# Optimization experiments

Hardware: AMD Instinct MI355X
Metric: run time of the kernel (lower is better)

The kernel has to match this reference:

```python
import jax, jax.numpy as jnp
import numpy as np

N_LVL = [131072, 32768, 8192, 2048, 512, 256]  # active voxels per pyramid level
B = 8          # point clouds in batch
K = 27         # 3x3x3 kernel offsets
SLOPE = 0.01   # LeakyReLU default negative slope
EPS = 1e-5     # BatchNorm eps


def _bn(x, g, b):
    # MinkowskiBatchNorm, training-mode forward: stats over all points
    m = x.mean(0)
    v = x.var(0)
    return (x - m) * jax.lax.rsqrt(v + EPS) * g + b


def _lrelu(x):
    return jnp.where(x >= 0, x, SLOPE * x)


def _lin_block(x, w, g, b):
    # MinkowskiLinear(bias=False) + BN + LeakyReLU (also models 1x1 conv)
    return _lrelu(_bn(x @ w, g, b))


def _conv_block(x, nbr, w, g, b):
    # sparse conv as gather-GEMM: [N,K,Cin] x [K,Cin,Cout] -> [N,Cout]
    y = jnp.einsum('nkc,kco->no', x[nbr], w)
    return _lrelu(_bn(y, g, b))


def _maxpool(x, pmap):
    # stride-2 kernel-3 sparse max pool via precomputed pooling map
    return x[pmap].max(axis=1)


def setup_inputs() -> dict:
    key = jax.random.key(0)
    ks = iter(jax.random.split(key, 80))

    def nrm(shape, scale):
        return jax.random.normal(next(ks), shape, dtype=jnp.float32) * jnp.float32(scale)

    inp = {}
    inp['x'] = nrm((N_LVL[0], 3), 1.0)
    inp['w_mlp1'] = nrm((3, 16), 1.0 / np.sqrt(3.0))
    inp['g_mlp1'] = jnp.ones(16, jnp.float32)
    inp['b_mlp1'] = jnp.zeros(16, jnp.float32)
    conv_dims = [(16, 32), (32, 48), (48, 96), (96, 128), (128, 256), (256, 512)]
    down_dims = [(48, 32), (80, 48), (144, 96), (224, 128), (384, 256)]
    for i, (ci, co) in enumerate(conv_dims):
        inp[f'w_c{i+1}'] = nrm((K, ci, co), np.sqrt(2.0 / (K * co)))  # kaiming fan_out
        inp[f'g_c{i+1}'] = jnp.ones(co, jnp.float32)
        inp[f'b_c{i+1}'] = jnp.zeros(co, jnp.float32)
    for i, (ci, co) in enumerate(down_dims):
        inp[f'w_d{i+1}'] = nrm((ci, co), np.sqrt(2.0 / co))
        inp[f'g_d{i+1}'] = jnp.ones(co, jnp.float32)
        inp[f'b_d{i+1}'] = jnp.zeros(co, jnp.float32)
    inp['w_f1'] = nrm((1024, 512), 1.0 / 32.0)
    inp['g_f1'] = jnp.ones(512, jnp.float32)
    inp['b_f1'] = jnp.zeros(512, jnp.float32)
    inp['w_f2'] = nrm((512, 256), 1.0 / np.sqrt(512.0))
    inp['g_f2'] = jnp.ones(256, jnp.float32)
    inp['b_f2'] = jnp.zeros(256, jnp.float32)
    inp['w_f3'] = nrm((256, 20), 1.0 / 16.0)
    inp['bias_f3'] = jnp.zeros(20, jnp.float32)
    for i in range(6):
        inp[f'nbr{i}'] = jax.random.randint(next(ks), (N_LVL[i], K), 0, N_LVL[i], dtype=jnp.int32)
    for i in range(1, 6):
        inp[f'pool{i}'] = jax.random.randint(next(ks), (N_LVL[i], K), 0, N_LVL[i - 1], dtype=jnp.int32)
    inp['batch5'] = jnp.repeat(jnp.arange(B, dtype=jnp.int32), N_LVL[5] // B)
    return inp


def reference(x, w_mlp1, g_mlp1, b_mlp1,
              w_c1, g_c1, b_c1, w_c2, g_c2, b_c2, w_c3, g_c3, b_c3,
              w_c4, g_c4, b_c4, w_c5, g_c5, b_c5, w_c6, g_c6, b_c6,
              w_d1, g_d1, b_d1, w_d2, g_d2, b_d2, w_d3, g_d3, b_d3,
              w_d4, g_d4, b_d4, w_d5, g_d5, b_d5,
              w_f1, g_f1, b_f1, w_f2, g_f2, b_f2, w_f3, bias_f3,
              nbr0, nbr1, nbr2, nbr3, nbr4, nbr5,
              pool1, pool2, pool3, pool4, pool5, batch5):
    convs = [(w_c1, g_c1, b_c1), (w_c2, g_c2, b_c2), (w_c3, g_c3, b_c3),
             (w_c4, g_c4, b_c4), (w_c5, g_c5, b_c5)]
    downs = [(w_d1, g_d1, b_d1), (w_d2, g_d2, b_d2), (w_d3, g_d3, b_d3),
             (w_d4, g_d4, b_d4), (w_d5, g_d5, b_d5)]
    nbrs = [nbr0, nbr1, nbr2, nbr3, nbr4]
    pools = [pool1, pool2, pool3, pool4, pool5]

    y = _lin_block(x, w_mlp1, g_mlp1, b_mlp1)  # mlp1, level 0
    for i in range(5):  # fixed 5 conv/cat/down/pool stages (structural loop)
        out = _conv_block(y, nbrs[i], *convs[i])
        y = _lin_block(jnp.concatenate([y, out], axis=1), *downs[i])  # cat + down (1x1)
        y = _maxpool(y, pools[i])
    y = _conv_block(y, nbr5, w_c6, g_c6, b_c6)  # conv6 at level 5: [N5, 512]

    xmax = jax.ops.segment_max(y, batch5, num_segments=B)
    cnt = jax.ops.segment_sum(jnp.ones((y.shape[0], 1), y.dtype), batch5, num_segments=B)
    xavg = jax.ops.segment_sum(y, batch5, num_segments=B) / cnt
    z = jnp.concatenate([xmax, xavg], axis=1)  # [B, 1024]

    z = _lin_block(z, w_f1, g_f1, b_f1)  # dropout = identity (eval)
    z = _lin_block(z, w_f2, g_f2, b_f2)
    return z @ w_f3 + bias_f3  # [B, 20] logits
```

## Files before the change

kernel.cpp:

```cpp
#include <hip/hip_runtime.h>
#include <math.h>

#define BN_EPS 1e-5f


__device__ __forceinline__ void fma4(float s, const float4& w, float4& a) {
    a.x = fmaf(s, w.x, a.x);
    a.y = fmaf(s, w.y, a.y);
    a.z = fmaf(s, w.z, a.z);
    a.w = fmaf(s, w.w, a.w);
}

__device__ __forceinline__ float nlr(float x, float sc, float sh) {
    float t = fmaf(x, sc, sh);
    return fmaxf(t, 0.01f * t);
}

__device__ __forceinline__ void bn_coef(const float* __restrict__ sums,
                                        const float* __restrict__ g,
                                        const float* __restrict__ b,
                                        int C, int c, float inv_n,
                                        float& sc, float& sh) {
    float mean = sums[c] * inv_n;
    float var = fmaxf(fmaf(-mean, mean, sums[C + c] * inv_n), 0.f);
    sc = g[c] * rsqrtf(var + BN_EPS);
    sh = fmaf(-mean, sc, b[c]);
}

__global__ void zero_kernel(float* __restrict__ p, int n) {
    int i = blockIdx.x * blockDim.x + threadIdx.x;
    if (i < n) p[i] = 0.f;
}

__global__ void mlp1_kernel(const float* __restrict__ x, const float* __restrict__ w,
                            float* __restrict__ out, int N) {
    int n = blockIdx.x * blockDim.x + threadIdx.x;
    if (n >= N) return;
    float x0 = x[n * 3], x1 = x[n * 3 + 1], x2 = x[n * 3 + 2];
    #pragma unroll
    for (int c4 = 0; c4 < 4; c4++) {
        float4 w0 = *reinterpret_cast<const float4*>(w + 0 + c4 * 4);
        float4 w1 = *reinterpret_cast<const float4*>(w + 16 + c4 * 4);
        float4 w2 = *reinterpret_cast<const float4*>(w + 32 + c4 * 4);
        float4 o;
        o.x = fmaf(x0, w0.x, fmaf(x1, w1.x, x2 * w2.x));
        o.y = fmaf(x0, w0.y, fmaf(x1, w1.y, x2 * w2.y));
        o.z = fmaf(x0, w0.z, fmaf(x1, w1.z, x2 * w2.z));
        o.w = fmaf(x0, w0.w, fmaf(x1, w1.w, x2 * w2.w));
        *reinterpret_cast<float4*>(out + n * 16 + c4 * 4) = o;
    }
}

__global__ void stats4_kernel(const float4* __restrict__ x, int total4, int C, int C4,
                              float* __restrict__ sums) {
    __shared__ float ls[1024];
    int tid = threadIdx.x;
    for (int j = tid; j < 2 * C; j += blockDim.x) ls[j] = 0.f;
    __syncthreads();
    int stride = gridDim.x * blockDim.x;
    int i = blockIdx.x * blockDim.x + tid;
    int c4 = i % C4;
    float4 s = make_float4(0.f, 0.f, 0.f, 0.f);
    float4 q = make_float4(0.f, 0.f, 0.f, 0.f);
    for (; i < total4; i += stride) {
        float4 v = x[i];
        s.x += v.x; s.y += v.y; s.z += v.z; s.w += v.w;
        q.x = fmaf(v.x, v.x, q.x); q.y = fmaf(v.y, v.y, q.y);
        q.z = fmaf(v.z, v.z, q.z); q.w = fmaf(v.w, v.w, q.w);
    }
    int cb = c4 * 4;
    atomicAdd(&ls[cb + 0], s.x); atomicAdd(&ls[cb + 1], s.y);
    atomicAdd(&ls[cb + 2], s.z); atomicAdd(&ls[cb + 3], s.w);
    atomicAdd(&ls[C + cb + 0], q.x); atomicAdd(&ls[C + cb + 1], q.y);
    atomicAdd(&ls[C + cb + 2], q.z); atomicAdd(&ls[C + cb + 3], q.w);
    __syncthreads();
    for (int j = tid; j < 2 * C; j += blockDim.x) atomicAdd(&sums[j], ls[j]);
}

template <int C, int KS>
__global__ __launch_bounds__(256) void reducek_kernel(
    const float4* __restrict__ in, float4* __restrict__ out, int total4,
    float* __restrict__ sums) {
    __shared__ float ls[1024];
    constexpr int C4 = C / 4;
    int tid = threadIdx.x;
    for (int j = tid; j < 2 * C; j += blockDim.x) ls[j] = 0.f;
    __syncthreads();
    int stride = gridDim.x * blockDim.x;
    int i = blockIdx.x * blockDim.x + tid;
    int c4 = i % C4;
    float4 s = make_float4(0.f, 0.f, 0.f, 0.f);
    float4 q = make_float4(0.f, 0.f, 0.f, 0.f);
    for (; i < total4; i += stride) {
        float4 v = make_float4(0.f, 0.f, 0.f, 0.f);
        #pragma unroll
        for (int p = 0; p < KS; p++) {
            float4 t = in[(size_t)p * total4 + i];
            v.x += t.x; v.y += t.y; v.z += t.z; v.w += t.w;
        }
        out[i] = v;
        s.x += v.x; s.y += v.y; s.z += v.z; s.w += v.w;
        q.x = fmaf(v.x, v.x, q.x); q.y = fmaf(v.y, v.y, q.y);
        q.z = fmaf(v.z, v.z, q.z); q.w = fmaf(v.w, v.w, q.w);
    }
    int cb = c4 * 4;
    atomicAdd(&ls[cb + 0], s.x); atomicAdd(&ls[cb + 1], s.y);
    atomicAdd(&ls[cb + 2], s.z); atomicAdd(&ls[cb + 3], s.w);
    atomicAdd(&ls[C + cb + 0], q.x); atomicAdd(&ls[C + cb + 1], q.y);
    atomicAdd(&ls[C + cb + 2], q.z); atomicAdd(&ls[C + cb + 3], q.w);
    __syncthreads();
    for (int j = tid; j < 2 * C; j += blockDim.x) atomicAdd(&sums[j], ls[j]);
}

template <int CIN, int COUT, int CO_TILE, int NCOT, int MT, int TM, int NTHR,
          int NQ, int KT, bool NORM_IN, bool STATS>
__global__ __launch_bounds__(NTHR) void convd_kernel(
    const float* __restrict__ y, const int* __restrict__ nbr,
    const float* __restrict__ w, float* __restrict__ out,
    const float* __restrict__ s_in, const float* __restrict__ g_in,
    const float* __restrict__ b_in, float inv_n,
    float* __restrict__ s_out) {
    constexpr int CQT = CO_TILE / (4 * NQ);
    constexpr int MGRP = NTHR / CQT;
    constexpr int RT = TM / MGRP;
    static_assert(MGRP * RT == TM, "tile mismatch");

    __shared__ float nsc[NORM_IN ? CIN : 1];
    __shared__ float nsh[NORM_IN ? CIN : 1];
    __shared__ float sred[STATS ? 2 * CO_TILE : 1];

    const int tid = threadIdx.x;
    const int bid = blockIdx.x;
    const int cot = bid % NCOT;
    const int rest = bid / NCOT;
    const int mt = rest % MT;
    const int ks = rest / MT;
    const int m0 = mt * TM;
    const int cobase = cot * CO_TILE;
    const int k0 = ks * KT;
    const int cq = tid % CQT;
    const int mg = tid / CQT;

    if constexpr (NORM_IN) {
        for (int c = tid; c < CIN; c += NTHR) {
            float sc, sh;
            bn_coef(s_in, g_in, b_in, CIN, c, inv_n, sc, sh);
            nsc[c] = sc;
            nsh[c] = sh;
        }
        __syncthreads();
    }

    int mrow[RT];
    #pragma unroll
    for (int r = 0; r < RT; r++) mrow[r] = m0 + mg + r * MGRP;

    float4 acc[RT][NQ];
    #pragma unroll
    for (int r = 0; r < RT; r++)
        #pragma unroll
        for (int q = 0; q < NQ; q++) acc[r][q] = make_float4(0.f, 0.f, 0.f, 0.f);

    for (int kk = k0; kk < k0 + KT; kk++) {
        int rows[RT];
        #pragma unroll
        for (int r = 0; r < RT; r++) rows[r] = nbr[(size_t)mrow[r] * 27 + kk];
        const float* wk = w + (size_t)kk * CIN * COUT + cobase + cq * (4 * NQ);
        #pragma unroll 4
        for (int ci4 = 0; ci4 < CIN / 4; ci4++) {
            float4 yv[RT];
            #pragma unroll
            for (int r = 0; r < RT; r++)
                yv[r] = *reinterpret_cast<const float4*>(
                    y + (size_t)rows[r] * CIN + ci4 * 4);
            if constexpr (NORM_IN) {
                float4 sc = *reinterpret_cast<const float4*>(&nsc[ci4 * 4]);
                float4 sh = *reinterpret_cast<const float4*>(&nsh[ci4 * 4]);
                #pragma unroll
                for (int r = 0; r < RT; r++) {
                    yv[r].x = nlr(yv[r].x, sc.x, sh.x);
                    yv[r].y = nlr(yv[r].y, sc.y, sh.y);
                    yv[r].z = nlr(yv[r].z, sc.z, sh.z);
                    yv[r].w = nlr(yv[r].w, sc.w, sh.w);
                }
            }
            #pragma unroll
            for (int jj = 0; jj < 4; jj++) {
                #pragma unroll
                for (int q = 0; q < NQ; q++) {
                    float4 wv = *reinterpret_cast<const float4*>(
                        wk + (size_t)(ci4 * 4 + jj) * COUT + q * 4);
                    #pragma unroll
                    for (int r = 0; r < RT; r++) {
                        float e = jj == 0 ? yv[r].x : jj == 1 ? yv[r].y
                                 : jj == 2 ? yv[r].z : yv[r].w;
                        fma4(e, wv, acc[r][q]);
                    }
                }
            }
        }
    }

    float* outp = out + (size_t)ks * MT * TM * COUT;
    #pragma unroll
    for (int r = 0; r < RT; r++)
        #pragma unroll
        for (int q = 0; q < NQ; q++)
            *reinterpret_cast<float4*>(
                outp + (size_t)mrow[r] * COUT + cobase + cq * (4 * NQ) + q * 4) =
                acc[r][q];

    if constexpr (STATS) {
        for (int j = tid; j < 2 * CO_TILE; j += NTHR) sred[j] = 0.f;
        __syncthreads();
        #pragma unroll
        for (int q = 0; q < NQ; q++) {
            float4 s = make_float4(0.f, 0.f, 0.f, 0.f);
            float4 qq = make_float4(0.f, 0.f, 0.f, 0.f);
            #pragma unroll
            for (int r = 0; r < RT; r++) {
                float4 v = acc[r][q];
                s.x += v.x; s.y += v.y; s.z += v.z; s.w += v.w;
                qq.x = fmaf(v.x, v.x, qq.x); qq.y = fmaf(v.y, v.y, qq.y);
                qq.z = fmaf(v.z, v.z, qq.z); qq.w = fmaf(v.w, v.w, qq.w);
            }
            int cb = cq * (4 * NQ) + q * 4;
            atomicAdd(&sred[cb + 0], s.x); atomicAdd(&sred[cb + 1], s.y);
            atomicAdd(&sred[cb + 2], s.z); atomicAdd(&sred[cb + 3], s.w);
            atomicAdd(&sred[CO_TILE + cb + 0], qq.x);
            atomicAdd(&sred[CO_TILE + cb + 1], qq.y);
            atomicAdd(&sred[CO_TILE + cb + 2], qq.z);
            atomicAdd(&sred[CO_TILE + cb + 3], qq.w);
        }
        __syncthreads();
        for (int j = tid; j < CO_TILE; j += NTHR) {
            atomicAdd(&s_out[cobase + j], sred[j]);
            atomicAdd(&s_out[COUT + cobase + j], sred[CO_TILE + j]);
        }
    }
}

template <int C1, int C2, int COUT, int NQ, int NTHR, bool NORM1>
__global__ __launch_bounds__(NTHR) void down3_kernel(
    const float* __restrict__ in1, const float* __restrict__ in2,
    const float* __restrict__ w, float* __restrict__ out,
    const float* __restrict__ s1, const float* __restrict__ g1,
    const float* __restrict__ b1, float inv1,
    const float* __restrict__ s2, const float* __restrict__ g2,
    const float* __restrict__ b2, float inv2,
    float* __restrict__ s_out) {
    constexpr int CQT = COUT / (4 * NQ);
    constexpr int PAIRS = NTHR / CQT;
    __shared__ __align__(16) float n1c[C1], n1h[C1], n2c[C2], n2h[C2];
    __shared__ float sred[2 * COUT];

    const int tid = threadIdx.x;
    if constexpr (NORM1) {
        for (int c = tid; c < C1; c += NTHR) {
            float sc, sh;
            bn_coef(s1, g1, b1, C1, c, inv1, sc, sh);
            n1c[c] = sc; n1h[c] = sh;
        }
    }
    for (int c = tid; c < C2; c += NTHR) {
        float sc, sh;
        bn_coef(s2, g2, b2, C2, c, inv2, sc, sh);
        n2c[c] = sc; n2h[c] = sh;
    }
    for (int j = tid; j < 2 * COUT; j += NTHR) sred[j] = 0.f;
    __syncthreads();

    const int cq = tid % CQT;
    const int pr = tid / CQT;
    const int n0 = (blockIdx.x * PAIRS + pr) * 2;

    float4 acc[2][NQ];
    #pragma unroll
    for (int r = 0; r < 2; r++)
        #pragma unroll
        for (int q = 0; q < NQ; q++) acc[r][q] = make_float4(0.f, 0.f, 0.f, 0.f);

    const float* w1 = w + cq * (4 * NQ);
    #pragma unroll 8
    for (int ci4 = 0; ci4 < C1 / 4; ci4++) {
        float4 a0 = *reinterpret_cast<const float4*>(in1 + (size_t)n0 * C1 + ci4 * 4);
        float4 a1 = *reinterpret_cast<const float4*>(in1 + (size_t)(n0 + 1) * C1 + ci4 * 4);
        if constexpr (NORM1) {
            float4 sc = *reinterpret_cast<const float4*>(&n1c[ci4 * 4]);
            float4 sh = *reinterpret_cast<const float4*>(&n1h[ci4 * 4]);
            a0.x = nlr(a0.x, sc.x, sh.x); a0.y = nlr(a0.y, sc.y, sh.y);
            a0.z = nlr(a0.z, sc.z, sh.z); a0.w = nlr(a0.w, sc.w, sh.w);
            a1.x = nlr(a1.x, sc.x, sh.x); a1.y = nlr(a1.y, sc.y, sh.y);
            a1.z = nlr(a1.z, sc.z, sh.z); a1.w = nlr(a1.w, sc.w, sh.w);
        }
        #pragma unroll
        for (int jj = 0; jj < 4; jj++) {
            const float* wp = w1 + (size_t)(ci4 * 4 + jj) * COUT;
            float e0 = jj == 0 ? a0.x : jj == 1 ? a0.y : jj == 2 ? a0.z : a0.w;
            float e1 = jj == 0 ? a1.x : jj == 1 ? a1.y : jj == 2 ? a1.z : a1.w;
            #pragma unroll
            for (int q = 0; q < NQ; q++) {
                float4 wv = *reinterpret_cast<const float4*>(wp + q * 4);
                fma4(e0, wv, acc[0][q]);
                fma4(e1, wv, acc[1][q]);
            }
        }
    }
    const float* w2 = w + (size_t)C1 * COUT + cq * (4 * NQ);
    #pragma unroll 8
    for (int ci4 = 0; ci4 < C2 / 4; ci4++) {
        float4 a0 = *reinterpret_cast<const float4*>(in2 + (size_t)n0 * C2 + ci4 * 4);
        float4 a1 = *reinterpret_cast<const float4*>(in2 + (size_t)(n0 + 1) * C2 + ci4 * 4);
        float4 sc = *reinterpret_cast<const float4*>(&n2c[ci4 * 4]);
        float4 sh = *reinterpret_cast<const float4*>(&n2h[ci4 * 4]);
        a0.x = nlr(a0.x, sc.x, sh.x); a0.y = nlr(a0.y, sc.y, sh.y);
        a0.z = nlr(a0.z, sc.z, sh.z); a0.w = nlr(a0.w, sc.w, sh.w);
        a1.x = nlr(a1.x, sc.x, sh.x); a1.y = nlr(a1.y, sc.y, sh.y);
        a1.z = nlr(a1.z, sc.z, sh.z); a1.w = nlr(a1.w, sc.w, sh.w);
        #pragma unroll
        for (int jj = 0; jj < 4; jj++) {
            const float* wp = w2 + (size_t)(ci4 * 4 + jj) * COUT;
            float e0 = jj == 0 ? a0.x : jj == 1 ? a0.y : jj == 2 ? a0.z : a0.w;
            float e1 = jj == 0 ? a1.x : jj == 1 ? a1.y : jj == 2 ? a1.z : a1.w;
            #pragma unroll
            for (int q = 0; q < NQ; q++) {
                float4 wv = *reinterpret_cast<const float4*>(wp + q * 4);
                fma4(e0, wv, acc[0][q]);
                fma4(e1, wv, acc[1][q]);
            }
        }
    }
    #pragma unroll
    for (int r = 0; r < 2; r++)
        #pragma unroll
        for (int q = 0; q < NQ; q++)
            *reinterpret_cast<float4*>(out + (size_t)(n0 + r) * COUT + cq * (4 * NQ) + q * 4) =
                acc[r][q];

    #pragma unroll
    for (int q = 0; q < NQ; q++) {
        float4 s = make_float4(0.f, 0.f, 0.f, 0.f);
        float4 qq = make_float4(0.f, 0.f, 0.f, 0.f);
        #pragma unroll
        for (int r = 0; r < 2; r++) {
            float4 v = acc[r][q];
            s.x += v.x; s.y += v.y; s.z += v.z; s.w += v.w;
            qq.x = fmaf(v.x, v.x, qq.x); qq.y = fmaf(v.y, v.y, qq.y);
            qq.z = fmaf(v.z, v.z, qq.z); qq.w = fmaf(v.w, v.w, qq.w);
        }
        int cb = cq * (4 * NQ) + q * 4;
        atomicAdd(&sred[cb + 0], s.x); atomicAdd(&sred[cb + 1], s.y);
        atomicAdd(&sred[cb + 2], s.z); atomicAdd(&sred[cb + 3], s.w);
        atomicAdd(&sred[COUT + cb + 0], qq.x);
        atomicAdd(&sred[COUT + cb + 1], qq.y);
        atomicAdd(&sred[COUT + cb + 2], qq.z);
        atomicAdd(&sred[COUT + cb + 3], qq.w);
    }
    __syncthreads();
    for (int j = tid; j < COUT; j += NTHR) {
        atomicAdd(&s_out[j], sred[j]);
        atomicAdd(&s_out[COUT + j], sred[COUT + j]);
    }
}

template <int C, int NTHR>
__global__ __launch_bounds__(NTHR) void pool2_kernel(
    const float* __restrict__ draw, const int* __restrict__ pmap,
    const float* __restrict__ sums, const float* __restrict__ g,
    const float* __restrict__ b, float inv_n,
    float* __restrict__ yout, int Nout) {
    constexpr int C4 = C / 4;
    int i = blockIdx.x * NTHR + threadIdx.x;
    if (i >= Nout * C4) return;
    int n = i / C4, c4 = i % C4;
    float sc[4], sh[4];
    #pragma unroll
    for (int j = 0; j < 4; j++) bn_coef(sums, g, b, C, c4 * 4 + j, inv_n, sc[j], sh[j]);
// ... 94 lines not shown
        red[kg * 520 + (coq * 4 + 2) * 8 + n] = acc[n].z;
        red[kg * 520 + (coq * 4 + 3) * 8 + n] = acc[n].w;
    }
    __syncthreads();
    for (int oi = tid; oi < 512; oi += 256) {
        int c = oi >> 3;
        int n = oi & 7;
        float s = 0.f;
        #pragma unroll
        for (int gg = 0; gg < 16; gg++) s += red[gg * 520 + c * 8 + n];
        float* op = out + (size_t)n * COUT + cobase + c;
        if (KSPLIT > 1) atomicAdd(op, s);
        else *op = s;
    }
}

__global__ void f3n_kernel(const float* __restrict__ in, const float* __restrict__ w,
                           const float* __restrict__ bias,
                           const float* __restrict__ sums, const float* __restrict__ g,
                           const float* __restrict__ b, float inv_n,
                           float* __restrict__ out) {
    __shared__ float zin[8 * 256];
    int tid = threadIdx.x;
    for (int idx = tid; idx < 2048; idx += 256) {
        int c = idx & 255;
        float sc, sh;
        bn_coef(sums, g, b, 256, c, inv_n, sc, sh);
        zin[idx] = nlr(in[idx], sc, sh);
    }
    __syncthreads();
    if (tid >= 160) return;
    int n = tid / 20, co = tid % 20;
    float acc = bias[co];
    for (int ci = 0; ci < 256; ci++)
        acc = fmaf(zin[n * 256 + ci], w[ci * 20 + co], acc);
    out[tid] = acc;
}


extern "C" void kernel_launch(void* const* d_in, const int* in_sizes, int n_in,
                              void* d_out, int out_size, void* d_ws, size_t ws_size,
                              hipStream_t stream) {
    (void)in_sizes; (void)n_in; (void)out_size; (void)ws_size;

    const int N0 = 131072, N1 = 32768, N2 = 8192, N3 = 2048, N4 = 512, N5 = 256;

    const float* x      = (const float*)d_in[0];
    const float* w_mlp1 = (const float*)d_in[1];
    const float* g_mlp1 = (const float*)d_in[2];
    const float* b_mlp1 = (const float*)d_in[3];
    const float* w_c[6]; const float* g_c[6]; const float* b_c[6];
    for (int i = 0; i < 6; i++) {
        w_c[i] = (const float*)d_in[4 + 3 * i];
        g_c[i] = (const float*)d_in[5 + 3 * i];
        b_c[i] = (const float*)d_in[6 + 3 * i];
    }
    const float* w_d[5]; const float* g_d[5]; const float* b_d[5];
    for (int i = 0; i < 5; i++) {
        w_d[i] = (const float*)d_in[22 + 3 * i];
        g_d[i] = (const float*)d_in[23 + 3 * i];
        b_d[i] = (const float*)d_in[24 + 3 * i];
    }
    const float* w_f1 = (const float*)d_in[37];
    const float* g_f1 = (const float*)d_in[38];
    const float* b_f1 = (const float*)d_in[39];
    const float* w_f2 = (const float*)d_in[40];
    const float* g_f2 = (const float*)d_in[41];
    const float* b_f2 = (const float*)d_in[42];
    const float* w_f3 = (const float*)d_in[43];
    const float* bias_f3 = (const float*)d_in[44];
    const int* nbr[6];
    for (int i = 0; i < 6; i++) nbr[i] = (const int*)d_in[45 + i];
    const int* pool[5];
    for (int i = 0; i < 5; i++) pool[i] = (const int*)d_in[51 + i];

    float* ws    = (float*)d_ws;
    float* bufA  = ws;
    float* bufB  = bufA + 2097152;
    float* bufC  = bufB + 4194304;
    float* stats = bufC + 4194304;
    float* out = (float*)d_out;

    auto st = [&](int slot) { return stats + slot * 1024; };
    auto run_stats = [&](const float* buf, int total, int C, int bs, int slot) {
        int total4 = total / 4, C4 = C / 4;
        int gr = (total4 + bs - 1) / bs;
        if (gr > 768) gr = 768;
        stats4_kernel<<<gr, bs, 0, stream>>>((const float4*)buf, total4, C, C4, st(slot));
    };

    const float iN0 = 1.f / N0, iN1 = 1.f / N1, iN2 = 1.f / N2, iN3 = 1.f / N3,
                iN4 = 1.f / N4, iN5 = 1.f / N5, i8 = 1.f / 8.f;

    zero_kernel<<<56, 256, 0, stream>>>(stats, 14 * 1024);

    mlp1_kernel<<<N0 / 256, 256, 0, stream>>>(x, w_mlp1, bufA, N0);
    run_stats(bufA, N0 * 16, 16, 256, 0);

    convd_kernel<16, 32, 32, 1, 1024, 128, 256, 2, 27, true, true>
        <<<1024, 256, 0, stream>>>(bufA, nbr[0], w_c[0], bufB,
                                   st(0), g_mlp1, b_mlp1, iN0, st(1));
    down3_kernel<16, 32, 32, 2, 256, true>
        <<<1024, 256, 0, stream>>>(bufA, bufB, w_d[0], bufC,
                                   st(0), g_mlp1, b_mlp1, iN0,
                                   st(1), g_c[0], b_c[0], iN0, st(2));
    pool2_kernel<32, 256><<<N1 * 8 / 256, 256, 0, stream>>>(
        bufC, pool[0], st(2), g_d[0], b_d[0], iN0, bufA, N1);

    convd_kernel<32, 48, 48, 1, 512, 64, 192, 2, 27, false, true>
        <<<512, 192, 0, stream>>>(bufA, nbr[1], w_c[1], bufB,
                                  nullptr, nullptr, nullptr, 0.f, st(3));
    down3_kernel<32, 48, 48, 2, 192, false>
        <<<512, 192, 0, stream>>>(bufA, bufB, w_d[1], bufC,
                                  nullptr, nullptr, nullptr, 0.f,
                                  st(3), g_c[1], b_c[1], iN1, st(4));
    pool2_kernel<48, 192><<<N2 * 12 / 192, 192, 0, stream>>>(
        bufC, pool[1], st(4), g_d[1], b_d[1], iN1, bufA, N2);

    convd_kernel<48, 96, 48, 2, 128, 64, 192, 2, 27, false, true>
        <<<256, 192, 0, stream>>>(bufA, nbr[2], w_c[2], bufB,
                                  nullptr, nullptr, nullptr, 0.f, st(5));
    down3_kernel<48, 96, 96, 2, 192, false>
        <<<256, 192, 0, stream>>>(bufA, bufB, w_d[2], bufC,
                                  nullptr, nullptr, nullptr, 0.f,
                                  st(5), g_c[2], b_c[2], iN2, st(6));
    pool2_kernel<96, 192><<<N3 * 24 / 192, 192, 0, stream>>>(
        bufC, pool[2], st(6), g_d[2], b_d[2], iN2, bufA, N3);

    convd_kernel<96, 128, 64, 2, 32, 64, 256, 2, 3, false, false>
        <<<576, 256, 0, stream>>>(bufA, nbr[3], w_c[3], bufC,
                                  nullptr, nullptr, nullptr, 0.f, nullptr);
    reducek_kernel<128, 9><<<256, 256, 0, stream>>>(
        (const float4*)bufC, (float4*)bufB, N3 * 32, st(7));
    down3_kernel<96, 128, 128, 2, 256, false>
        <<<64, 256, 0, stream>>>(bufA, bufB, w_d[3], bufC,
                                 nullptr, nullptr, nullptr, 0.f,
                                 st(7), g_c[3], b_c[3], iN3, st(8));
    pool2_kernel<128, 256><<<N4 * 32 / 256, 256, 0, stream>>>(
        bufC, pool[3], st(8), g_d[3], b_d[3], iN3, bufA, N4);

    convd_kernel<128, 256, 64, 4, 8, 64, 256, 2, 3, false, false>
        <<<288, 256, 0, stream>>>(bufA, nbr[4], w_c[4], bufC,
                                  nullptr, nullptr, nullptr, 0.f, nullptr);
    reducek_kernel<256, 9><<<128, 256, 0, stream>>>(
        (const float4*)bufC, (float4*)bufB, N4 * 64, st(9));
    down3_kernel<128, 256, 256, 2, 256, false>
        <<<32, 256, 0, stream>>>(bufA, bufB, w_d[4], bufC,
                                 nullptr, nullptr, nullptr, 0.f,
                                 st(9), g_c[4], b_c[4], iN4, st(10));
    pool2_kernel<256, 256><<<N5 * 64 / 256, 256, 0, stream>>>(
        bufC, pool[4], st(10), g_d[4], b_d[4], iN4, bufA, N5);

    convd_kernel<256, 512, 64, 8, 4, 64, 256, 2, 1, false, false>
        <<<864, 256, 0, stream>>>(bufA, nbr[5], w_c[5], bufC,
                                  nullptr, nullptr, nullptr, 0.f, nullptr);
    reducek_kernel<512, 27><<<128, 256, 0, stream>>>(
        (const float4*)bufC, (float4*)bufB, N5 * 128, st(11));

    segpool2_kernel<<<8, 512, 0, stream>>>(bufB, st(11), g_c[5], b_c[5], iN5, bufC);

    zero_kernel<<<16, 256, 0, stream>>>(bufA, 4096);
    fc_kernel<1024, 512, 4, false><<<dim3(8, 4), 256, 0, stream>>>(
        bufC, w_f1, nullptr, nullptr, nullptr, 0.f, bufA);
    run_stats(bufA, 8 * 512, 512, 256, 12);

    zero_kernel<<<8, 256, 0, stream>>>(bufB, 2048);
    fc_kernel<512, 256, 4, true><<<dim3(4, 4), 256, 0, stream>>>(
        bufA, w_f2, st(12), g_f1, b_f1, i8, bufB);
    run_stats(bufB, 8 * 256, 256, 256, 13);

    f3n_kernel<<<1, 256, 0, stream>>>(bufB, w_f3, bias_f3, st(13), g_f2, b_f2, i8, out);
}
```

Before: 1.148 ms.

## Split-K sparse convs more widely and double-buffer gathers in first conv

The level-1 and level-2 convolutions now split the 27 kernel offsets across more blocks, writing per-split partial outputs that a reducek kernel sums while also computing BN statistics. The deeper convolutions move to one offset per block with a 27-way reduction, done in place in bufB. The first convolution gains a prefetch path that loads the next offset's gathered rows while FMAs run on the current ones. Neighbour indices are also loaded one offset ahead. The aim is more parallelism on under-occupied layers and hidden gather latency, at the cost of extra partial-sum memory traffic and larger intermediate buffers.

After: 1.055 ms. -8.2%, faster.

```diff
diff --git a/kernel.cpp b/kernel.cpp
--- a/kernel.cpp
+++ b/kernel.cpp
@@ -78,9 +78,8 @@
 }
 
 template <int C, int KS>
-__global__ __launch_bounds__(256) void reducek_kernel(
-    const float4* __restrict__ in, float4* __restrict__ out, int total4,
-    float* __restrict__ sums) {
+__global__ void reducek_kernel(const float4* __restrict__ in, float4* __restrict__ out,
+                               int total4, float* __restrict__ sums) {
     __shared__ float ls[1024];
     constexpr int C4 = C / 4;
     int tid = threadIdx.x;
@@ -113,7 +112,7 @@
 }
 
 template <int CIN, int COUT, int CO_TILE, int NCOT, int MT, int TM, int NTHR,
-          int NQ, int KT, bool NORM_IN, bool STATS>
+          int NQ, int KT, bool NORM_IN, bool STATS, bool PREF>
 __global__ __launch_bounds__(NTHR) void convd_kernel(
     const float* __restrict__ y, const int* __restrict__ nbr,
     const float* __restrict__ w, float* __restrict__ out,
@@ -123,7 +122,9 @@
     constexpr int CQT = CO_TILE / (4 * NQ);
     constexpr int MGRP = NTHR / CQT;
     constexpr int RT = TM / MGRP;
+    constexpr int C4N = CIN / 4;
     static_assert(MGRP * RT == TM, "tile mismatch");
+    static_assert(MGRP * CQT == NTHR, "thread mismatch");
 
     __shared__ float nsc[NORM_IN ? CIN : 1];
     __shared__ float nsh[NORM_IN ? CIN : 1];
@@ -148,7 +149,6 @@
             nsc[c] = sc;
             nsh[c] = sh;
         }
-        __syncthreads();
     }
 
     int mrow[RT];
@@ -161,43 +161,93 @@
         #pragma unroll
         for (int q = 0; q < NQ; q++) acc[r][q] = make_float4(0.f, 0.f, 0.f, 0.f);
 
-    for (int kk = k0; kk < k0 + KT; kk++) {
-        int rows[RT];
-        #pragma unroll
-        for (int r = 0; r < RT; r++) rows[r] = nbr[(size_t)mrow[r] * 27 + kk];
-        const float* wk = w + (size_t)kk * CIN * COUT + cobase + cq * (4 * NQ);
-        #pragma unroll 4
-        for (int ci4 = 0; ci4 < CIN / 4; ci4++) {
-            float4 yv[RT];
-            #pragma unroll
-            for (int r = 0; r < RT; r++)
-                yv[r] = *reinterpret_cast<const float4*>(
-                    y + (size_t)rows[r] * CIN + ci4 * 4);
-            if constexpr (NORM_IN) {
-                float4 sc = *reinterpret_cast<const float4*>(&nsc[ci4 * 4]);
-                float4 sh = *reinterpret_cast<const float4*>(&nsh[ci4 * 4]);
+    auto ldidx = [&](int k, int (&rr)[RT]) {
+        #pragma unroll
+        for (int r = 0; r < RT; r++) rr[r] = nbr[(size_t)mrow[r] * 27 + k];
+    };
+    auto fma_ci4 = [&](const float* wk, int ci4, float4 (&yv)[RT]) {
+        if constexpr (NORM_IN) {
+            float4 sc = *reinterpret_cast<const float4*>(&nsc[ci4 * 4]);
+            float4 sh = *reinterpret_cast<const float4*>(&nsh[ci4 * 4]);
+            #pragma unroll
+            for (int r = 0; r < RT; r++) {
+                yv[r].x = nlr(yv[r].x, sc.x, sh.x);
+                yv[r].y = nlr(yv[r].y, sc.y, sh.y);
+                yv[r].z = nlr(yv[r].z, sc.z, sh.z);
+                yv[r].w = nlr(yv[r].w, sc.w, sh.w);
+            }
+        }
+        #pragma unroll
+        for (int jj = 0; jj < 4; jj++) {
+            #pragma unroll
+            for (int q = 0; q < NQ; q++) {
+                float4 wv = *reinterpret_cast<const float4*>(
+                    wk + (size_t)(ci4 * 4 + jj) * COUT + q * 4);
                 #pragma unroll
                 for (int r = 0; r < RT; r++) {
-                    yv[r].x = nlr(yv[r].x, sc.x, sh.x);
-                    yv[r].y = nlr(yv[r].y, sc.y, sh.y);
-                    yv[r].z = nlr(yv[r].z, sc.z, sh.z);
-                    yv[r].w = nlr(yv[r].w, sc.w, sh.w);
+                    float e = jj == 0 ? yv[r].x : jj == 1 ? yv[r].y
+                             : jj == 2 ? yv[r].z : yv[r].w;
+                    fma4(e, wv, acc[r][q]);
                 }
             }
-            #pragma unroll
-            for (int jj = 0; jj < 4; jj++) {
+        }
+    };
+
+    if constexpr (PREF) {
+        auto ldy = [&](const int (&rr)[RT], float4 (&yv)[RT][C4N]) {
+            #pragma unroll
+            for (int r = 0; r < RT; r++)
                 #pragma unroll
-                for (int q = 0; q < NQ; q++) {
-                    float4 wv = *reinterpret_cast<const float4*>(
-                        wk + (size_t)(ci4 * 4 + jj) * COUT + q * 4);
-                    #pragma unroll
-                    for (int r = 0; r < RT; r++) {
-                        float e = jj == 0 ? yv[r].x : jj == 1 ? yv[r].y
-                                 : jj == 2 ? yv[r].z : yv[r].w;
-                        fma4(e, wv, acc[r][q]);
-                    }
-                }
-            }
+                for (int c4 = 0; c4 < C4N; c4++)
+                    yv[r][c4] = *reinterpret_cast<const float4*>(
+                        y + (size_t)rr[r] * CIN + c4 * 4);
+        };
+        auto fmak = [&](int k, float4 (&yv)[RT][C4N]) {
+            const float* wk = w + (size_t)k * CIN * COUT + cobase + cq * (4 * NQ);
+            #pragma unroll
+            for (int ci4 = 0; ci4 < C4N; ci4++) {
+                float4 col[RT];
+                #pragma unroll
+                for (int r = 0; r < RT; r++) col[r] = yv[r][ci4];
+                fma_ci4(wk, ci4, col);
+            }
+        };
+        int ra[RT], rb[RT];
+        float4 ya[RT][C4N], yb[RT][C4N];
+        ldidx(k0, ra);
+        ldy(ra, ya);
+        if constexpr (NORM_IN) __syncthreads();
+        int kk = 0;
+        for (; kk + 2 <= KT; kk += 2) {
+            ldidx(k0 + kk + 1, rb);
+            ldy(rb, yb);
+            fmak(k0 + kk, ya);
+            if (kk + 2 < KT) {
+                ldidx(k0 + kk + 2, ra);
+                ldy(ra, ya);
+            }
+            fmak(k0 + kk + 1, yb);
+        }
+        if (KT & 1) fmak(k0 + KT - 1, ya);
+    } else {
+        if constexpr (NORM_IN) __syncthreads();
+        int rows[RT];
+        ldidx(k0, rows);
+        for (int kk = k0; kk < k0 + KT; kk++) {
+            int rnext[RT];
+            if (kk + 1 < k0 + KT) ldidx(kk + 1, rnext);
+            const float* wk = w + (size_t)kk * CIN * COUT + cobase + cq * (4 * NQ);
+            #pragma unroll 4
+            for (int ci4 = 0; ci4 < C4N; ci4++) {
+                float4 yv[RT];
+                #pragma unroll
+                for (int r = 0; r < RT; r++)
+                    yv[r] = *reinterpret_cast<const float4*>(
+                        y + (size_t)rows[r] * CIN + ci4 * 4);
+                fma_ci4(wk, ci4, yv);
+            }
+            #pragma unroll
+            for (int r = 0; r < RT; r++) rows[r] = rnext[r];
         }
     }
 
@@ -568,7 +618,7 @@
     mlp1_kernel<<<N0 / 256, 256, 0, stream>>>(x, w_mlp1, bufA, N0);
     run_stats(bufA, N0 * 16, 16, 256, 0);
 
-    convd_kernel<16, 32, 32, 1, 1024, 128, 256, 2, 27, true, true>
+    convd_kernel<16, 32, 32, 1, 1024, 128, 256, 2, 27, true, true, true>
         <<<1024, 256, 0, stream>>>(bufA, nbr[0], w_c[0], bufB,
                                    st(0), g_mlp1, b_mlp1, iN0, st(1));
     down3_kernel<16, 32, 32, 2, 256, true>
@@ -578,9 +628,11 @@
     pool2_kernel<32, 256><<<N1 * 8 / 256, 256, 0, stream>>>(
         bufC, pool[0], st(2), g_d[0], b_d[0], iN0, bufA, N1);
 
-    convd_kernel<32, 48, 48, 1, 512, 64, 192, 2, 27, false, true>
-        <<<512, 192, 0, stream>>>(bufA, nbr[1], w_c[1], bufB,
-                                  nullptr, nullptr, nullptr, 0.f, st(3));
+    convd_kernel<32, 48, 48, 1, 512, 64, 192, 2, 9, false, false, false>
+        <<<1536, 192, 0, stream>>>(bufA, nbr[1], w_c[1], bufB,
+                                   nullptr, nullptr, nullptr, 0.f, nullptr);
+    reducek_kernel<48, 3><<<1024, 192, 0, stream>>>(
+        (const float4*)bufB, (float4*)bufB, N1 * 12, st(3));
     down3_kernel<32, 48, 48, 2, 192, false>
         <<<512, 192, 0, stream>>>(bufA, bufB, w_d[1], bufC,
                                   nullptr, nullptr, nullptr, 0.f,
@@ -588,9 +640,11 @@
     pool2_kernel<48, 192><<<N2 * 12 / 192, 192, 0, stream>>>(
         bufC, pool[1], st(4), g_d[1], b_d[1], iN1, bufA, N2);
 
-    convd_kernel<48, 96, 48, 2, 128, 64, 192, 2, 27, false, true>
-        <<<256, 192, 0, stream>>>(bufA, nbr[2], w_c[2], bufB,
-                                  nullptr, nullptr, nullptr, 0.f, st(5));
+    convd_kernel<48, 96, 48, 2, 128, 64, 192, 2, 3, false, false, false>
+        <<<2304, 192, 0, stream>>>(bufA, nbr[2], w_c[2], bufB,
+                                   nullptr, nullptr, nullptr, 0.f, nullptr);
+    reducek_kernel<96, 9><<<1024, 192, 0, stream>>>(
+        (const float4*)bufB, (float4*)bufB, N2 * 24, st(5));
     down3_kernel<48, 96, 96, 2, 192, false>
         <<<256, 192, 0, stream>>>(bufA, bufB, w_d[2], bufC,
                                   nullptr, nullptr, nullptr, 0.f,
@@ -598,11 +652,11 @@
     pool2_kernel<96, 192><<<N3 * 24 / 192, 192, 0, stream>>>(
         bufC, pool[2], st(6), g_d[2], b_d[2], iN2, bufA, N3);
 
-    convd_kernel<96, 128, 64, 2, 32, 64, 256, 2, 3, false, false>
-        <<<576, 256, 0, stream>>>(bufA, nbr[3], w_c[3], bufC,
-                                  nullptr, nullptr, nullptr, 0.f, nullptr);
-    reducek_kernel<128, 9><<<256, 256, 0, stream>>>(
-        (const float4*)bufC, (float4*)bufB, N3 * 32, st(7));
+    convd_kernel<96, 128, 64, 2, 32, 64, 256, 2, 1, false, false, false>
+        <<<1728, 256, 0, stream>>>(bufA, nbr[3], w_c[3], bufB,
+                                   nullptr, nullptr, nullptr, 0.f, nullptr);
+    reducek_kernel<128, 27><<<256, 256, 0, stream>>>(
+        (const float4*)bufB, (float4*)bufB, N3 * 32, st(7));
     down3_kernel<96, 128, 128, 2, 256, false>
         <<<64, 256, 0, stream>>>(bufA, bufB, w_d[3], bufC,
                                  nullptr, nullptr, nullptr, 0.f,
@@ -610,11 +664,11 @@
     pool2_kernel<128, 256><<<N4 * 32 / 256, 256, 0, stream>>>(
         bufC, pool[3], st(8), g_d[3], b_d[3], iN3, bufA, N4);
 
-    convd_kernel<128, 256, 64, 4, 8, 64, 256, 2, 3, false, false>
-        <<<288, 256, 0, stream>>>(bufA, nbr[4], w_c[4], bufC,
+    convd_kernel<128, 256, 64, 4, 8, 64, 256, 2, 1, false, false, false>
+        <<<864, 256, 0, stream>>>(bufA, nbr[4], w_c[4], bufB,
                                   nullptr, nullptr, nullptr, 0.f, nullptr);
-    reducek_kernel<256, 9><<<128, 256, 0, stream>>>(
-        (const float4*)bufC, (float4*)bufB, N4 * 64, st(9));
+    reducek_kernel<256, 27><<<128, 256, 0, stream>>>(
+        (const float4*)bufB, (float4*)bufB, N4 * 64, st(9));
     down3_kernel<128, 256, 256, 2, 256, false>
         <<<32, 256, 0, stream>>>(bufA, bufB, w_d[4], bufC,
                                  nullptr, nullptr, nullptr, 0.f,
@@ -622,11 +676,11 @@
     pool2_kernel<256, 256><<<N5 * 64 / 256, 256, 0, stream>>>(
         bufC, pool[4], st(10), g_d[4], b_d[4], iN4, bufA, N5);
 
-    convd_kernel<256, 512, 64, 8, 4, 64, 256, 2, 1, false, false>
-        <<<864, 256, 0, stream>>>(bufA, nbr[5], w_c[5], bufC,
+    convd_kernel<256, 512, 64, 8, 4, 64, 256, 2, 1, false, false, false>
+        <<<864, 256, 0, stream>>>(bufA, nbr[5], w_c[5], bufB,
                                   nullptr, nullptr, nullptr, 0.f, nullptr);
     reducek_kernel<512, 27><<<128, 256, 0, stream>>>(
-        (const float4*)bufC, (float4*)bufB, N5 * 128, st(11));
+        (const float4*)bufB, (float4*)bufB, N5 * 128, st(11));
 
     segpool2_kernel<<<8, 512, 0, stream>>>(bufB, st(11), g_c[5], b_c[5], iN5, bufC);
 
```

## Split-K and retile sparse convs, add prefetched gather path, pre-normalize level-0 features

Applied to the files above, without the earlier changes.

Level-0 features are now normalized in place by a new norm0 kernel, so the conv and down kernels no longer apply BN and LeakyReLU on the fly. A PREF path in the conv kernel preloads the neighbour indices and double-buffers whole input rows in registers across kernel offsets. All conv launches are retiled to smaller row tiles with more blocks. Conv2 and conv3 become split-K launches followed by an in-place reducek reduction, which also computes the BN statistics. The aim is more parallelism and better latency hiding on the gather-GEMMs, at the cost of extra partial-sum traffic, extra launches and higher register pressure from the row buffers.

Result: slower. 1.495 ms (+30.2%).

```diff
diff --git a/kernel.cpp b/kernel.cpp
--- a/kernel.cpp
+++ b/kernel.cpp
@@ -77,10 +77,32 @@
     for (int j = tid; j < 2 * C; j += blockDim.x) atomicAdd(&sums[j], ls[j]);
 }
 
+__global__ void norm0_kernel(float4* __restrict__ y, int total4,
+                             const float* __restrict__ sums, const float* __restrict__ g,
+                             const float* __restrict__ b, float inv_n) {
+    __shared__ float lsc[16], lsh[16];
+    int tid = threadIdx.x;
+    if (tid < 16) {
+        float sc, sh;
+        bn_coef(sums, g, b, 16, tid, inv_n, sc, sh);
+        lsc[tid] = sc;
+        lsh[tid] = sh;
+    }
+    __syncthreads();
+    int i = blockIdx.x * blockDim.x + tid;
+    if (i >= total4) return;
+    int cb = (i & 3) * 4;
+    float4 v = y[i];
+    v.x = nlr(v.x, lsc[cb + 0], lsh[cb + 0]);
+    v.y = nlr(v.y, lsc[cb + 1], lsh[cb + 1]);
+    v.z = nlr(v.z, lsc[cb + 2], lsh[cb + 2]);
+    v.w = nlr(v.w, lsc[cb + 3], lsh[cb + 3]);
+    y[i] = v;
+}
+
 template <int C, int KS>
-__global__ __launch_bounds__(256) void reducek_kernel(
-    const float4* __restrict__ in, float4* __restrict__ out, int total4,
-    float* __restrict__ sums) {
+__global__ void reducek_kernel(const float4* __restrict__ in, float4* __restrict__ out,
+                               int total4, float* __restrict__ sums) {
     __shared__ float ls[1024];
     constexpr int C4 = C / 4;
     int tid = threadIdx.x;
@@ -113,20 +135,19 @@
 }
 
 template <int CIN, int COUT, int CO_TILE, int NCOT, int MT, int TM, int NTHR,
-          int NQ, int KT, bool NORM_IN, bool STATS>
+          int NQ, int KT, bool STATS, bool PREF>
 __global__ __launch_bounds__(NTHR) void convd_kernel(
     const float* __restrict__ y, const int* __restrict__ nbr,
     const float* __restrict__ w, float* __restrict__ out,
-    const float* __restrict__ s_in, const float* __restrict__ g_in,
-    const float* __restrict__ b_in, float inv_n,
     float* __restrict__ s_out) {
     constexpr int CQT = CO_TILE / (4 * NQ);
     constexpr int MGRP = NTHR / CQT;
     constexpr int RT = TM / MGRP;
+    constexpr int C4N = CIN / 4;
     static_assert(MGRP * RT == TM, "tile mismatch");
-
-    __shared__ float nsc[NORM_IN ? CIN : 1];
-    __shared__ float nsh[NORM_IN ? CIN : 1];
+    static_assert(MGRP * CQT == NTHR, "thread mismatch");
+    static_assert(!PREF || RT == 1, "PREF requires RT==1");
+
     __shared__ float sred[STATS ? 2 * CO_TILE : 1];
 
     const int tid = threadIdx.x;
@@ -141,63 +162,91 @@
     const int cq = tid % CQT;
     const int mg = tid / CQT;
 
-    if constexpr (NORM_IN) {
-        for (int c = tid; c < CIN; c += NTHR) {
-            float sc, sh;
-            bn_coef(s_in, g_in, b_in, CIN, c, inv_n, sc, sh);
-            nsc[c] = sc;
-            nsh[c] = sh;
-        }
-        __syncthreads();
-    }
-
-    int mrow[RT];
-    #pragma unroll
-    for (int r = 0; r < RT; r++) mrow[r] = m0 + mg + r * MGRP;
-
     float4 acc[RT][NQ];
     #pragma unroll
     for (int r = 0; r < RT; r++)
         #pragma unroll
         for (int q = 0; q < NQ; q++) acc[r][q] = make_float4(0.f, 0.f, 0.f, 0.f);
 
-    for (int kk = k0; kk < k0 + KT; kk++) {
+    if constexpr (PREF) {
+        const int mrow = m0 + mg;
+        int idxs[KT];
+        #pragma unroll
+        for (int kk = 0; kk < KT; kk++)
+            idxs[kk] = nbr[(size_t)mrow * 27 + k0 + kk];
+
+        auto ldy = [&](int row, float4 (&yv)[C4N]) {
+            #pragma unroll
+            for (int c4 = 0; c4 < C4N; c4++)
+                yv[c4] = *reinterpret_cast<const float4*>(
+                    y + (size_t)row * CIN + c4 * 4);
+        };
+        auto fmak = [&](int k, const float4 (&yv)[C4N]) {
+            const float* wk = w + (size_t)k * CIN * COUT + cobase + cq * (4 * NQ);
+            #pragma unroll
+            for (int c4 = 0; c4 < C4N; c4++) {
+                #pragma unroll
+                for (int jj = 0; jj < 4; jj++) {
+                    float e = jj == 0 ? yv[c4].x : jj == 1 ? yv[c4].y
+                             : jj == 2 ? yv[c4].z : yv[c4].w;
+                    #pragma unroll
+                    for (int q = 0; q < NQ; q++) {
+                        float4 wv = *reinterpret_cast<const float4*>(
+                            wk + (size_t)(c4 * 4 + jj) * COUT + q * 4);
+                        fma4(e, wv, acc[0][q]);
+                    }
+                }
+            }
+        };
+        float4 ya[C4N], yb[C4N];
+        ldy(idxs[0], ya);
+        int kk = 0;
+        for (; kk + 2 <= KT; kk += 2) {
+            ldy(idxs[kk + 1], yb);
+            fmak(k0 + kk, ya);
+            if (kk + 2 < KT) ldy(idxs[kk + 2], ya);
+            fmak(k0 + kk + 1, yb);
+        }
+        if (KT & 1) fmak(k0 + KT - 1, ya);
+    } else {
+        int mrow[RT];
+        #pragma unroll
+        for (int r = 0; r < RT; r++) mrow[r] = m0 + mg + r * MGRP;
         int rows[RT];
         #pragma unroll
-        for (int r = 0; r < RT; r++) rows[r] = nbr[(size_t)mrow[r] * 27 + kk];
-        const float* wk = w + (size_t)kk * CIN * COUT + cobase + cq * (4 * NQ);
-        #pragma unroll 4
-        for (int ci4 = 0; ci4 < CIN / 4; ci4++) {
-            float4 yv[RT];
-            #pragma unroll
-            for (int r = 0; r < RT; r++)
-                yv[r] = *reinterpret_cast<const float4*>(
-                    y + (size_t)rows[r] * CIN + ci4 * 4);
-            if constexpr (NORM_IN) {
-                float4 sc = *reinterpret_cast<const float4*>(&nsc[ci4 * 4]);
-                float4 sh = *reinterpret_cast<const float4*>(&nsh[ci4 * 4]);
+        for (int r = 0; r < RT; r++) rows[r] = nbr[(size_t)mrow[r] * 27 + k0];
+        for (int kk = k0; kk < k0 + KT; kk++) {
+            int rnext[RT];
+            if (kk + 1 < k0 + KT) {
                 #pragma unroll
-                for (int r = 0; r < RT; r++) {
-                    yv[r].x = nlr(yv[r].x, sc.x, sh.x);
-                    yv[r].y = nlr(yv[r].y, sc.y, sh.y);
-                    yv[r].z = nlr(yv[r].z, sc.z, sh.z);
-                    yv[r].w = nlr(yv[r].w, sc.w, sh.w);
+                for (int r = 0; r < RT; r++)
+                    rnext[r] = nbr[(size_t)mrow[r] * 27 + kk + 1];
+            }
+            const float* wk = w + (size_t)kk * CIN * COUT + cobase + cq * (4 * NQ);
+            #pragma unroll 4
+            for (int c4 = 0; c4 < C4N; c4++) {
+                float4 yv[RT];
+                #pragma unroll
+                for (int r = 0; r < RT; r++)
+                    yv[r] = *reinterpret_cast<const float4*>(
+                        y + (size_t)rows[r] * CIN + c4 * 4);
+                #pragma unroll
+                for (int jj = 0; jj < 4; jj++) {
+                    #pragma unroll
+                    for (int q = 0; q < NQ; q++) {
+                        float4 wv = *reinterpret_cast<const float4*>(
+                            wk + (size_t)(c4 * 4 + jj) * COUT + q * 4);
+                        #pragma unroll
+                        for (int r = 0; r < RT; r++) {
+                            float e = jj == 0 ? yv[r].x : jj == 1 ? yv[r].y
+                                     : jj == 2 ? yv[r].z : yv[r].w;
+                            fma4(e, wv, acc[r][q]);
+                        }
+                    }
                 }
             }
             #pragma unroll
-            for (int jj = 0; jj < 4; jj++) {
-                #pragma unroll
-                for (int q = 0; q < NQ; q++) {
-                    float4 wv = *reinterpret_cast<const float4*>(
-                        wk + (size_t)(ci4 * 4 + jj) * COUT + q * 4);
-                    #pragma unroll
-                    for (int r = 0; r < RT; r++) {
-                        float e = jj == 0 ? yv[r].x : jj == 1 ? yv[r].y
-                                 : jj == 2 ? yv[r].z : yv[r].w;
-                        fma4(e, wv, acc[r][q]);
-                    }
-                }
-            }
+            for (int r = 0; r < RT; r++) rows[r] = rnext[r];
         }
     }
 
@@ -207,7 +256,7 @@
         #pragma unroll
         for (int q = 0; q < NQ; q++)
             *reinterpret_cast<float4*>(
-                outp + (size_t)mrow[r] * COUT + cobase + cq * (4 * NQ) + q * 4) =
+                outp + (size_t)(m0 + mg + r * MGRP) * COUT + cobase + cq * (4 * NQ) + q * 4) =
                 acc[r][q];
 
     if constexpr (STATS) {
@@ -240,28 +289,19 @@
     }
 }
 
-template <int C1, int C2, int COUT, int NQ, int NTHR, bool NORM1>
+template <int C1, int C2, int COUT, int NQ, int NTHR>
 __global__ __launch_bounds__(NTHR) void down3_kernel(
     const float* __restrict__ in1, const float* __restrict__ in2,
     const float* __restrict__ w, float* __restrict__ out,
-    const float* __restrict__ s1, const float* __restrict__ g1,
-    const float* __restrict__ b1, float inv1,
     const float* __restrict__ s2, const float* __restrict__ g2,
     const float* __restrict__ b2, float inv2,
     float* __restrict__ s_out) {
     constexpr int CQT = COUT / (4 * NQ);
     constexpr int PAIRS = NTHR / CQT;
-    __shared__ __align__(16) float n1c[C1], n1h[C1], n2c[C2], n2h[C2];
+    __shared__ __align__(16) float n2c[C2], n2h[C2];
     __shared__ float sred[2 * COUT];
 
     const int tid = threadIdx.x;
-    if constexpr (NORM1) {
-        for (int c = tid; c < C1; c += NTHR) {
-            float sc, sh;
-            bn_coef(s1, g1, b1, C1, c, inv1, sc, sh);
-            n1c[c] = sc; n1h[c] = sh;
-        }
-    }
     for (int c = tid; c < C2; c += NTHR) {
         float sc, sh;
         bn_coef(s2, g2, b2, C2, c, inv2, sc, sh);
@@ -285,14 +325,6 @@
     for (int ci4 = 0; ci4 < C1 / 4; ci4++) {
         float4 a0 = *reinterpret_cast<const float4*>(in1 + (size_t)n0 * C1 + ci4 * 4);
         float4 a1 = *reinterpret_cast<const float4*>(in1 + (size_t)(n0 + 1) * C1 + ci4 * 4);
-        if constexpr (NORM1) {
-            float4 sc = *reinterpret_cast<const float4*>(&n1c[ci4 * 4]);
-            float4 sh = *reinterpret_cast<const float4*>(&n1h[ci4 * 4]);
-            a0.x = nlr(a0.x, sc.x, sh.x); a0.y = nlr(a0.y, sc.y, sh.y);
-            a0.z = nlr(a0.z, sc.z, sh.z); a0.w = nlr(a0.w, sc.w, sh.w);
-            a1.x = nlr(a1.x, sc.x, sh.x); a1.y = nlr(a1.y, sc.y, sh.y);
-            a1.z = nlr(a1.z, sc.z, sh.z); a1.w = nlr(a1.w, sc.w, sh.w);
-        }
         #pragma unroll
         for (int jj = 0; jj < 4; jj++) {
             const float* wp = w1 + (size_t)(ci4 * 4 + jj) * COUT;
@@ -553,12 +585,6 @@
     float* out = (float*)d_out;
 
     auto st = [&](int slot) { return stats + slot * 1024; };
-    auto run_stats = [&](const float* buf, int total, int C, int bs, int slot) {
-        int total4 = total / 4, C4 = C / 4;
-        int gr = (total4 + bs - 1) / bs;
-        if (gr > 768) gr = 768;
-        stats4_kernel<<<gr, bs, 0, stream>>>((const float4*)buf, total4, C, C4, st(slot));
-    };
 
     const float iN0 = 1.f / N0, iN1 = 1.f / N1, iN2 = 1.f / N2, iN3 = 1.f / N3,
                 iN4 = 1.f / N4, iN5 = 1.f / N5, i8 = 1.f / 8.f;
@@ -566,79 +592,76 @@
     zero_kernel<<<56, 256, 0, stream>>>(stats, 14 * 1024);
 
     mlp1_kernel<<<N0 / 256, 256, 0, stream>>>(x, w_mlp1, bufA, N0);
-    run_stats(bufA, N0 * 16, 16, 256, 0);
-
-    convd_kernel<16, 32, 32, 1, 1024, 128, 256, 2, 27, true, true>
-        <<<1024, 256, 0, stream>>>(bufA, nbr[0], w_c[0], bufB,
-                                   st(0), g_mlp1, b_mlp1, iN0, st(1));
-    down3_kernel<16, 32, 32, 2, 256, true>
+    stats4_kernel<<<768, 256, 0, stream>>>((const float4*)bufA, N0 * 4, 16, 4, st(0));
+    norm0_kernel<<<N0 * 4 / 256, 256, 0, stream>>>(
+        (float4*)bufA, N0 * 4, st(0), g_mlp1, b_mlp1, iN0);
+
+    convd_kernel<16, 32, 32, 1, 2048, 64, 256, 2, 27, true, true>
+        <<<2048, 256, 0, stream>>>(bufA, nbr[0], w_c[0], bufB, st(1));
+    down3_kernel<16, 32, 32, 2, 256>
         <<<1024, 256, 0, stream>>>(bufA, bufB, w_d[0], bufC,
-                                   st(0), g_mlp1, b_mlp1, iN0,
                                    st(1), g_c[0], b_c[0], iN0, st(2));
     pool2_kernel<32, 256><<<N1 * 8 / 256, 256, 0, stream>>>(
         bufC, pool[0], st(2), g_d[0], b_d[0], iN0, bufA, N1);
 
-    convd_kernel<32, 48, 48, 1, 512, 64, 192, 2, 27, false, true>
-        <<<512, 192, 0, stream>>>(bufA, nbr[1], w_c[1], bufB,
-                                  nullptr, nullptr, nullptr, 0.f, st(3));
-    down3_kernel<32, 48, 48, 2, 192, false>
+    convd_kernel<32, 48, 48, 1, 1024, 32, 192, 2, 9, false, true>
+        <<<3072, 192, 0, stream>>>(bufA, nbr[1], w_c[1], bufB, nullptr);
+    reducek_kernel<48, 3><<<1024, 192, 0, stream>>>(
+        (const float4*)bufB, (float4*)bufB, N1 * 12, st(3));
+    down3_kernel<32, 48, 48, 2, 192>
         <<<512, 192, 0, stream>>>(bufA, bufB, w_d[1], bufC,
-                                  nullptr, nullptr, nullptr, 0.f,
                                   st(3), g_c[1], b_c[1], iN1, st(4));
     pool2_kernel<48, 192><<<N2 * 12 / 192, 192, 0, stream>>>(
         bufC, pool[1], st(4), g_d[1], b_d[1], iN1, bufA, N2);
 
-    convd_kernel<48, 96, 48, 2, 128, 64, 192, 2, 27, false, true>
-        <<<256, 192, 0, stream>>>(bufA, nbr[2], w_c[2], bufB,
-                                  nullptr, nullptr, nullptr, 0.f, st(5));
-    down3_kernel<48, 96, 96, 2, 192, false>
+    convd_kernel<48, 96, 48, 2, 256, 32, 192, 2, 9, false, false>
+        <<<1536, 192, 0, stream>>>(bufA, nbr[2], w_c[2], bufB, nullptr);
+    reducek_kernel<96, 3><<<1024, 192, 0, stream>>>(
+        (const float4*)bufB, (float4*)bufB, N2 * 24, st(5));
+    down3_kernel<48, 96, 96, 2, 192>
         <<<256, 192, 0, stream>>>(bufA, bufB, w_d[2], bufC,
-                                  nullptr, nullptr, nullptr, 0.f,
                                   st(5), g_c[2], b_c[2], iN2, st(6));
     pool2_kernel<96, 192><<<N3 * 24 / 192, 192, 0, stream>>>(
         bufC, pool[2], st(6), g_d[2], b_d[2], iN2, bufA, N3);
 
-    convd_kernel<96, 128, 64, 2, 32, 64, 256, 2, 3, false, false>
-        <<<576, 256, 0, stream>>>(bufA, nbr[3], w_c[3], bufC,
-                                  nullptr, nullptr, nullptr, 0.f, nullptr);
+    convd_kernel<96, 128, 64, 2, 64, 32, 256, 2, 3, false, false>
+        <<<1152, 256, 0, stream>>>(bufA, nbr[3], w_c[3], bufB, nullptr);
     reducek_kernel<128, 9><<<256, 256, 0, stream>>>(
-        (const float4*)bufC, (float4*)bufB, N3 * 32, st(7));
-    down3_kernel<96, 128, 128, 2, 256, false>
+        (const float4*)bufB, (float4*)bufB, N3 * 32, st(7));
+    down3_kernel<96, 128, 128, 2, 256>
         <<<64, 256, 0, stream>>>(bufA, bufB, w_d[3], bufC,
-                                 nullptr, nullptr, nullptr, 0.f,
                                  st(7), g_c[3], b_c[3], iN3, st(8));
     pool2_kernel<128, 256><<<N4 * 32 / 256, 256, 0, stream>>>(
         bufC, pool[3], st(8), g_d[3], b_d[3], iN3, bufA, N4);
 
-    convd_kernel<128, 256, 64, 4, 8, 64, 256, 2, 3, false, false>
-        <<<288, 256, 0, stream>>>(bufA, nbr[4], w_c[4], bufC,
-                                  nullptr, nullptr, nullptr, 0.f, nullptr);
+    convd_kernel<128, 256, 64, 4, 16, 32, 256, 2, 3, false, false>
+        <<<576, 256, 0, stream>>>(bufA, nbr[4], w_c[4], bufB, nullptr);
     reducek_kernel<256, 9><<<128, 256, 0, stream>>>(
-        (const float4*)bufC, (float4*)bufB, N4 * 64, st(9));
-    down3_kernel<128, 256, 256, 2, 256, false>
+        (const float4*)bufB, (float4*)bufB, N4 * 64, st(9));
+    down3_kernel<128, 256, 256, 2, 256>
         <<<32, 256, 0, stream>>>(bufA, bufB, w_d[4], bufC,
-                                 nullptr, nullptr, nullptr, 0.f,
                                  st(9), g_c[4], b_c[4], iN4, st(10));
     pool2_kernel<256, 256><<<N5 * 64 / 256, 256, 0, stream>>>(
         bufC, pool[4], st(10), g_d[4], b_d[4], iN4, bufA, N5);
 
-    convd_kernel<256, 512, 64, 8, 4, 64, 256, 2, 1, false, false>
-        <<<864, 256, 0, stream>>>(bufA, nbr[5], w_c[5], bufC,
-                                  nullptr, nullptr, nullptr, 0.f, nullptr);
-    reducek_kernel<512, 27><<<128, 256, 0, stream>>>(
-        (const float4*)bufC, (float4*)bufB, N5 * 128, st(11));
+    convd_kernel<256, 512, 64, 8, 8, 32, 256, 2, 3, false, false>
+        <<<576, 256, 0, stream>>>(bufA, nbr[5], w_c[5], bufB, nullptr);
+    reducek_kernel<512, 9><<<128, 256, 0, stream>>>(
+        (const float4*)bufB, (float4*)bufB, N5 * 128, st(11));
 
     segpool2_kernel<<<8, 512, 0, stream>>>(bufB, st(11), g_c[5], b_c[5], iN5, bufC);
 
-    zero_kernel<<<16, 256, 0, stream>>>(bufA, 4096);
+    zero_kernel<<<16, 256, 0, stream>>>(bufB, 4096);
     fc_kernel<1024, 512, 4, false><<<dim3(8, 4), 256, 0, stream>>>(
-        bufC, w_f1, nullptr, nullptr, nullptr, 0.f, bufA);
-    run_stats(bufA, 8 * 512, 512, 256, 12);
-
-    zero_kernel<<<8, 256, 0, stream>>>(bufB, 2048);
+        bufC, w_f1, nullptr, nullptr, nullptr, 0.f, bufB);
+    stats4_kernel<<<4, 256, 0, stream>>>((const float4*)bufB, 1024, 512, 128, st(12));
+
+    zero_kernel<<<8, 256, 0, stream>>>(bufB + 4096, 2048);
     fc_kernel<512, 256, 4, true><<<dim3(4, 4), 256, 0, stream>>>(
-        bufA, w_f2, st(12), g_f1, b_f1, i8, bufB);
-    run_stats(bufB, 8 * 256, 256, 256, 13);
-
-    f3n_kernel<<<1, 256, 0, stream>>>(bufB, w_f3, bias_f3, st(13), g_f2, b_f2, i8, out);
-}
+        bufB, w_f2, st(12), g_f1, b_f1, i8, bufB + 4096);
+    stats4_kernel<<<2, 256, 0, stream>>>(
+        (const float4*)(bufB + 4096), 512, 256, 64, st(13));
+
+    f3n_kernel<<<1, 256, 0, stream>>>(bufB + 4096, w_f3, bias_f3,
+                                      st(13), g_f2, b_f2, i8, out);
+}
```
